# Kernel optimization log

Hardware: AMD Instinct MI355X
Metric: run time of the kernel (lower is better)

## Reference

```python
import jax, jax.numpy as jnp
import numpy as np

G = 32           # number of graphs
NODES = 256      # nodes per graph (equal-sized graphs)
P = 8            # primary capsules per node
IN_DIM = 128     # primary capsule dim
O = 16           # out_caps
OUT_DIM = 128    # out capsule dim
SDIM = OUT_DIM // 2
V = 16           # vector channels
R = 3            # routing iterations


def squash(t, axis=-1):
    sn = jnp.sum(t * t, axis=axis, keepdims=True)
    scale = sn / (1.0 + sn)
    return scale * t / (jnp.sqrt(sn) + 1e-8)


def setup_inputs() -> dict:
    key = jax.random.key(0)
    ks = jax.random.split(key, 4)
    N = G * NODES
    x = jax.random.normal(ks[0], (N, P, IN_DIM), dtype=jnp.float32)
    x_vectors = jax.random.normal(ks[1], (N, V, 3), dtype=jnp.float32)
    W_scalar = jax.random.normal(ks[2], (O, IN_DIM // 2, SDIM), dtype=jnp.float32)
    W_vector = jax.random.normal(ks[3], (O, IN_DIM // 2, OUT_DIM - SDIM), dtype=jnp.float32)
    bias = jnp.zeros((O, OUT_DIM), dtype=jnp.float32)
    batch = jnp.repeat(jnp.arange(G, dtype=jnp.int64), NODES)  # contiguous equal-size graphs
    return {"x": x, "x_vectors": x_vectors, "W_scalar": W_scalar,
            "W_vector": W_vector, "bias": bias, "batch": batch}


def reference(x, x_vectors, W_scalar, W_vector, bias, batch):
    # Equal-size contiguous graphs -> per-graph masking == reshape to [G, NODES, ...]
    xg = x.reshape(G, NODES, P, IN_DIM)
    xvg = x_vectors.reshape(G, NODES, V, 3)

    def per_graph(xb, xvb):
        scalar_part = xb[..., : IN_DIM // 2]           # [n, P, D/2]
        vector_part = xb[..., IN_DIM // 2:]
        u_s = jnp.einsum('npd,ods->npos', scalar_part, W_scalar)
        u_v = jnp.einsum('npd,odv->npov', vector_part, W_vector)
        u = jnp.concatenate([u_s, u_v], axis=-1).reshape(NODES * P, O, OUT_DIM)

        b = jnp.zeros((NODES * P, O), dtype=xb.dtype)
        c = None
        v = None
        for it in range(R):
            c = jax.nn.softmax(b, axis=1)                     # [M, O]
            s_j = jnp.einsum('mo,mod->od', c, u) + bias       # [O, OUT_DIM]
            v = squash(s_j, axis=1)
            if it < R - 1:
                agreement = jnp.einsum('mos,os->mo', u[..., :SDIM], v[:, :SDIM])
                b = b + agreement

        cr = c.reshape(NODES, P, O)
        routed = jnp.einsum('npo,nvc->ovc', cr, xvb)          # [O, V, 3]
        return v, routed

    caps, vecs = jax.vmap(per_graph)(xg, xvg)
    return caps, vecs
```

## Files before the change

kernel.cpp:

```cpp
#include <hip/hip_runtime.h>

#define G_    32
#define O_    16
#define OUTD  128
#define DS_   64
#define VC    48
#define M_    2048
#define ROWS  128
#define CPG   16
#define XP    136
#define XPD   68
#define WVP   72
#define YLP   132

typedef __attribute__((ext_vector_type(8))) short short8;
typedef __attribute__((ext_vector_type(4))) float f32x4;
typedef unsigned long long u64_t;

__device__ __forceinline__ unsigned short f2bf(float f) {
  unsigned u = __float_as_uint(f);
  return (unsigned short)((u + 0x7FFFu + ((u >> 16) & 1u)) >> 16);
}
__device__ __forceinline__ float bf2f(short v) {
  return __uint_as_float(((unsigned)(unsigned short)v) << 16);
}

__device__ __forceinline__ void st8f(float* p, float a, float b) {
  union { float f[2]; u64_t u; } x; x.f[0] = a; x.f[1] = b;
  __hip_atomic_store((u64_t*)p, x.u, __ATOMIC_RELAXED, __HIP_MEMORY_SCOPE_AGENT);
}
__device__ __forceinline__ void ld8f(const float* p, float& a, float& b) {
  union { float f[2]; u64_t u; } x;
  x.u = __hip_atomic_load((const u64_t*)p, __ATOMIC_RELAXED, __HIP_MEMORY_SCOPE_AGENT);
  a = x.f[0]; b = x.f[1];
}

__device__ __forceinline__ void graph_barrier(unsigned* cnt, unsigned target) {
  asm volatile("s_waitcnt vmcnt(0)" ::: "memory");
  __syncthreads();
  if (threadIdx.x == 0) {
    __hip_atomic_fetch_add(cnt, 1u, __ATOMIC_RELAXED, __HIP_MEMORY_SCOPE_AGENT);
    unsigned guard = 0;
    while (__hip_atomic_load(cnt, __ATOMIC_RELAXED, __HIP_MEMORY_SCOPE_AGENT) < target) {
      __builtin_amdgcn_s_sleep(1);
      if (++guard > (1u << 20)) break;
    }
  }
  __syncthreads();
}

__global__ __launch_bounds__(512) void caps_mega(
    const float* __restrict__ x, const float* __restrict__ xv,
    const float* __restrict__ Ws, const float* __restrict__ Wv,
    const float* __restrict__ bias, short* __restrict__ wvacc_bf,
    float* __restrict__ y_part, float* __restrict__ routed_part,
    float* __restrict__ ysum_part, float* __restrict__ caps,
    float* __restrict__ vecs, unsigned* __restrict__ bar)
{
  const int b = blockIdx.x, g = b >> 3, pair = b & 7;
  const int t = threadIdx.x, h = t >> 8, tt = t & 255;
  const int lane = tt & 63, w = tt >> 6;
  const int chunk = pair * 2 + h;
  const int blk_lin = g * CPG + chunk;

  __shared__ short xT[2][128 * XP];
  __shared__ short cT[2][O_ * XP];
  __shared__ short wv_s[O_ * WVP];
  __shared__ float y_lds[2][16 * YLP];
  __shared__ float cp_s[2][16][17];
  __shared__ float xv_s[2][16 * VC];
  __shared__ float yB[2][128];
  __shared__ float vB[2][64];
  __shared__ float pn_s[4];
  __shared__ float wv_acc_s[2][64];

  unsigned* cnt = bar + g * 64;

  {
    const float* xg = x + (size_t)(g * M_ + chunk * ROWS) * OUTD;
    const int rg = tt >> 2, qc = tt & 3;
    const float4* r0q = (const float4*)(xg + (size_t)(2 * rg) * OUTD + qc * 32);
    const float4* r1q = (const float4*)(xg + (size_t)(2 * rg + 1) * OUTD + qc * 32);
    float4 a0 = r0q[0], a1 = r0q[1], a2 = r0q[2], a3 = r0q[3],
           a4 = r0q[4], a5 = r0q[5], a6 = r0q[6], a7 = r0q[7];
    float4 b0 = r1q[0], b1 = r1q[1], b2 = r1q[2], b3 = r1q[3],
           b4 = r1q[4], b5 = r1q[5], b6 = r1q[6], b7 = r1q[7];
    unsigned* xTd = (unsigned*)&xT[h][0];
    const int cb = qc * 32;
#define STAGE4(S, A, B)                                                        \
    xTd[(cb + S*4 + 0) * XPD + rg] = (unsigned)f2bf(A.x) | ((unsigned)f2bf(B.x) << 16); \
    xTd[(cb + S*4 + 1) * XPD + rg] = (unsigned)f2bf(A.y) | ((unsigned)f2bf(B.y) << 16); \
    xTd[(cb + S*4 + 2) * XPD + rg] = (unsigned)f2bf(A.z) | ((unsigned)f2bf(B.z) << 16); \
    xTd[(cb + S*4 + 3) * XPD + rg] = (unsigned)f2bf(A.w) | ((unsigned)f2bf(B.w) << 16);
    STAGE4(0, a0, b0) STAGE4(1, a1, b1) STAGE4(2, a2, b2) STAGE4(3, a3, b3)
    STAGE4(4, a4, b4) STAGE4(5, a5, b5) STAGE4(6, a6, b6) STAGE4(7, a7, b7)
#undef STAGE4
  }
  {
    const float* xvg = xv + (size_t)(g * 256 + chunk * 16) * VC;
    for (int i = tt; i < 16 * VC; i += 256) xv_s[h][i] = xvg[i];
  }
  __syncthreads();
  {
    const int k = tt >> 1, half = tt & 1;
    float s = 0.f;
#pragma unroll
    for (int j = 0; j < 8; ++j) {
      short8 v = *(const short8*)&xT[h][k * XP + half * 64 + j * 8];
#pragma unroll
      for (int e = 0; e < 8; ++e) s += bf2f(v[e]);
    }
    s += __shfl_xor(s, 1);
    float s1 = __shfl_xor(s, 2);
    if ((tt & 3) == 0) st8f(&ysum_part[(size_t)blk_lin * 128 + k], s, s1);
  }
  graph_barrier(cnt, 8);

#define LOGIT_TILE(NT2, CF)                                                    \
    {                                                                          \
      const int nt = 2 * w + NT2;                                              \
      const int mcol = nt * 16 + mrow;                                         \
      f32x4 acc = {0.f, 0.f, 0.f, 0.f};                                        \
      _Pragma("unroll")                                                        \
      for (int ks = 0; ks < 2; ++ks) {                                         \
        short8 af = *(const short8*)&wv_s[mrow * WVP + ks * 32 + gq * 8];      \
        short8 bfr;                                                            \
        _Pragma("unroll")                                                      \
        for (int e = 0; e < 8; ++e)                                            \
          bfr[e] = xT[h][(ks * 32 + gq * 8 + e) * XP + mcol];                  \
        acc = __builtin_amdgcn_mfma_f32_16x16x32_bf16(af, bfr, acc, 0, 0, 0);  \
      }                                                                        \
      float mx = fmaxf(fmaxf(acc[0], acc[1]), fmaxf(acc[2], acc[3]));          \
      mx = fmaxf(mx, __shfl_xor(mx, 16));                                      \
      mx = fmaxf(mx, __shfl_xor(mx, 32));                                      \
      float e0 = __expf(acc[0] - mx), e1 = __expf(acc[1] - mx);                \
      float e2 = __expf(acc[2] - mx), e3 = __expf(acc[3] - mx);                \
      float sm = e0 + e1 + e2 + e3;                                            \
      sm += __shfl_xor(sm, 16);                                                \
      sm += __shfl_xor(sm, 32);                                                \
      float inv = 1.f / sm;                                                    \
      CF[0] = e0 * inv; CF[1] = e1 * inv; CF[2] = e2 * inv; CF[3] = e3 * inv;  \
      cT[h][(gq * 4 + 0) * XP + mcol] = (short)f2bf(CF[0]);                    \
      cT[h][(gq * 4 + 1) * XP + mcol] = (short)f2bf(CF[1]);                    \
      cT[h][(gq * 4 + 2) * XP + mcol] = (short)f2bf(CF[2]);                    \
      cT[h][(gq * 4 + 3) * XP + mcol] = (short)f2bf(CF[3]);                    \
    }

#define CP_TILE(NT2, CF)                                                       \
    {                                                                          \
      const int nt = 2 * w + NT2;                                              \
      _Pragma("unroll")                                                        \
      for (int r = 0; r < 4; ++r) {                                            \
        float v = CF[r];                                                       \
        v += __shfl_xor(v, 1); v += __shfl_xor(v, 2); v += __shfl_xor(v, 4);   \
        if ((lane & 7) == 0)                                                   \
          cp_s[h][nt * 2 + ((lane >> 3) & 1)][gq * 4 + r] = v;                 \
      }                                                                        \
    }

#define A_ROLE(LASTF)                                                          \
  {                                                                            \
    if (t < 256) {                                                             \
      u64_t v4 = __hip_atomic_load(                                            \
          (const u64_t*)&wvacc_bf[(size_t)g * 1024 + t * 4],                   \
          __ATOMIC_RELAXED, __HIP_MEMORY_SCOPE_AGENT);                         \
      const int o = (t * 4) >> 6, k = (t * 4) & 63;                            \
      wv_s[o * WVP + k + 0] = (short)(v4 & 0xFFFF);                            \
      wv_s[o * WVP + k + 1] = (short)((v4 >> 16) & 0xFFFF);                    \
      wv_s[o * WVP + k + 2] = (short)((v4 >> 32) & 0xFFFF);                    \
      wv_s[o * WVP + k + 3] = (short)((v4 >> 48) & 0xFFFF);                    \
    }                                                                          \
    __syncthreads();                                                           \
    { const int mrow = lane & 15, gq = lane >> 4;                              \
      float c_fA[4], c_fB[4];                                                  \
      LOGIT_TILE(0, c_fA)                                                      \
      LOGIT_TILE(1, c_fB)                                                      \
      if (LASTF) { CP_TILE(0, c_fA) CP_TILE(1, c_fB) }                         \
      (void)c_fA; (void)c_fB; }                                                \
    __syncthreads();                                                           \
    { const int oc = lane & 15, gq = lane >> 4;                                \
      f32x4 y0 = {0.f,0.f,0.f,0.f}, y1 = {0.f,0.f,0.f,0.f};                    \
      _Pragma("unroll")                                                        \
      for (int ks = 0; ks < 4; ++ks) {                                         \
        short8 bfv = *(const short8*)&cT[h][oc * XP + ks * 32 + gq * 8];       \
        short8 a0 = *(const short8*)&xT[h][((2*w+0)*16 + oc) * XP + ks*32 + gq*8]; \
        short8 a1 = *(const short8*)&xT[h][((2*w+1)*16 + oc) * XP + ks*32 + gq*8]; \
        y0 = __builtin_amdgcn_mfma_f32_16x16x32_bf16(a0, bfv, y0, 0, 0, 0);    \
        y1 = __builtin_amdgcn_mfma_f32_16x16x32_bf16(a1, bfv, y1, 0, 0, 0);    \
      }                                                                        \
      _Pragma("unroll")                                                        \
      for (int r = 0; r < 4; ++r) {                                            \
        y_lds[h][oc * YLP + (2*w+0) * 16 + gq * 4 + r] = y0[r];                \
        y_lds[h][oc * YLP + (2*w+1) * 16 + gq * 4 + r] = y1[r];                \
      } }                                                                      \
    __syncthreads();                                                           \
    { float* yp = y_part + (size_t)blk_lin * 2048;                             \
      const int oo = tt >> 4, k8 = (tt & 15) * 8;                              \
      const float* sp = &y_lds[h][oo * YLP + k8];                              \
      _Pragma("unroll")                                                        \
      for (int e = 0; e < 4; ++e)                                              \
        st8f(&yp[tt * 8 + 2*e], sp[2*e], sp[2*e + 1]); }                       \
    if (LASTF) {                                                               \
      float* rp = routed_part + (size_t)blk_lin * 768;                         \
      _Pragma("unroll")                                                        \
      for (int e = 0; e < 2; ++e) {                                            \
        const int q = tt + 256 * e;                                            \
        if (q < 384) {                                                         \
          const int idx0 = 2 * q;                                              \
          const int o = idx0 / VC, j = idx0 - o * VC;                          \
          float a0 = 0.f, a1 = 0.f;                                            \
          _Pragma("unroll")                                                    \
          for (int n = 0; n < 16; ++n) {                                       \
            a0 += cp_s[h][n][o] * xv_s[h][n * VC + j];                         \
            a1 += cp_s[h][n][o] * xv_s[h][n * VC + j + 1];                     \
          }                                                                    \
          st8f(&rp[idx0], a0, a1);                                             \
        } } }                                                                  \
  }

#define B_ROLE(FIRSTF, LASTF)                                                  \
  {                                                                            \
    if (FIRSTF) {                                                              \
      if (t < 64) {                                                            \
        float s0 = 0.f, s1 = 0.f;                                              \
        _Pragma("unroll")                                                      \
        for (int ch = 0; ch < CPG; ++ch) {                                     \
          float a, bb;                                                         \
          ld8f(&ysum_part[(size_t)(g * CPG + ch) * 128 + 2 * t], a, bb);       \
          s0 += a; s1 += bb;                                                   \
        }                                                                      \
        s0 *= 0.0625f; s1 *= 0.0625f;                                          \
        yB[0][2*t] = s0; yB[0][2*t+1] = s1;                                    \
        yB[1][2*t] = s0; yB[1][2*t+1] = s1;                                    \
      }                                                                        \
    } else {                                                                   \
      if (t < 128) {                                                           \
        const int o2 = t >> 6, kp = t & 63;                                    \
        const float* yp = y_part + (size_t)g * CPG * 2048 + (pair*2 + o2) * 128 + kp * 2; \
        float s0 = 0.f, s1 = 0.f;                                              \
        _Pragma("unroll")                                                      \
        for (int ch = 0; ch < CPG; ++ch) {                                     \
          float a, bb; ld8f(&yp[ch * 2048], a, bb);                            \
          s0 += a; s1 += bb;                                                   \
        }                                                                      \
        yB[o2][kp*2] = s0; yB[o2][kp*2+1] = s1;                                \
      }                                                                        \
    }                                                                          \
    __syncthreads();                                                           \
    float sv = 0.f;                                                            \
    if (t < 256) {                                                             \
      const int ol = t >> 7, d = t & 127, o = pair * 2 + ol;                   \
      const float* W = (d < 64) ? (Ws + (size_t)o * 4096 + d)                  \
                                : (Wv + (size_t)o * 4096 + (d - 64));          \
      const int kbase = (d < 64) ? 0 : 64;                                     \
      float s = 0.f;                                                           \
      _Pragma("unroll")                                                        \
      for (int k = 0; k < 64; ++k) s += yB[ol][kbase + k] * W[k * 64];         \
      s += bias[o * OUTD + d];                                                 \
      sv = s;                                                                  \
      float pn = s * s;                                                        \
      _Pragma("unroll")                                                        \
      for (int m = 1; m < 64; m <<= 1) pn += __shfl_xor(pn, m);                \
      if ((t & 63) == 0) pn_s[t >> 6] = pn;                                    \
    }                                                                          \
    __syncthreads();                                                           \
    if (t < 256) {                                                             \
      const int ol = t >> 7, d = t & 127, o = pair * 2 + ol;                   \
      float sn = pn_s[ol * 2] + pn_s[ol * 2 + 1];                              \
      float f = sn / ((1.f + sn) * (sqrtf(sn) + 1e-8f));                       \
      float v = f * sv;                                                        \
      if (d < 64) vB[ol][d] = v;                                               \
      if (LASTF) caps[((size_t)g * O_ + o) * OUTD + d] = v;                    \
    }                                                                          \
    __syncthreads();                                                           \
    if (!(LASTF)) {                                                            \
      if (t < 128) {                                                           \
        const int ol2 = t >> 6, k = t & 63, o2 = pair * 2 + ol2;               \
        const float* Wr = Ws + ((size_t)o2 * 64 + k) * 64;                     \
        float acc = 0.f;                                                       \
        _Pragma("unroll")                                                      \
        for (int ss = 0; ss < 64; ss += 4) {                                   \
          float4 wq = *(const float4*)(Wr + ss);                               \
          float4 vq = *(const float4*)&vB[ol2][ss];                            \
          acc += wq.x*vq.x + wq.y*vq.y + wq.z*vq.z + wq.w*vq.w;                \
        }                                                                      \
        wv_acc_s[ol2][k] = ((FIRSTF) ? 0.f : wv_acc_s[ol2][k]) + acc;          \
      }                                                                        \
      __syncthreads();                                                         \
      if (t < 32) {                                                            \
        const int ol2 = t >> 4, k = (t & 15) * 4;                              \
        u64_t v4 =  (u64_t)(unsigned short)f2bf(wv_acc_s[ol2][k + 0])          \
                 | ((u64_t)(unsigned short)f2bf(wv_acc_s[ol2][k + 1]) << 16)   \
                 | ((u64_t)(unsigned short)f2bf(wv_acc_s[ol2][k + 2]) << 32)   \
                 | ((u64_t)(unsigned short)f2bf(wv_acc_s[ol2][k + 3]) << 48);  \
        __hip_atomic_store(                                                    \
            (u64_t*)&wvacc_bf[(size_t)g * 1024 + (pair * 2 + ol2) * 64 + k],   \
            v4, __ATOMIC_RELAXED, __HIP_MEMORY_SCOPE_AGENT);                   \
      }                                                                        \
    } else {                                                                   \
      if (t < 48) {                                                            \
        const int idx = pair * 96 + 2 * t;                                     \
        const float* rp = routed_part + (size_t)g * CPG * 768 + idx;           \
        float s0 = 0.f, s1 = 0.f;                                              \
        _Pragma("unroll")                                                      \
        for (int ch = 0; ch < CPG; ++ch) {                                     \
          float a, bb; ld8f(&rp[ch * 768], a, bb);                             \
          s0 += a; s1 += bb;                                                   \
        }                                                                      \
        vecs[(size_t)g * 768 + idx] = s0;                                      \
        vecs[(size_t)g * 768 + idx + 1] = s1;                                  \
      }                                                                        \
    }                                                                          \
  }

  B_ROLE(1, 0)
  graph_barrier(cnt, 16);
  A_ROLE(0)
  graph_barrier(cnt, 24);
  B_ROLE(0, 0)
  graph_barrier(cnt, 32);
  A_ROLE(1)
  graph_barrier(cnt, 40);
  B_ROLE(0, 1)

#undef A_ROLE
#undef B_ROLE
#undef LOGIT_TILE
#undef CP_TILE
}

extern "C" void kernel_launch(void* const* d_in, const int* in_sizes, int n_in,
                              void* d_out, int out_size, void* d_ws, size_t ws_size,
                              hipStream_t stream)
{
  const float* x    = (const float*)d_in[0];
  const float* xv   = (const float*)d_in[1];
  const float* Ws   = (const float*)d_in[2];
  const float* Wv   = (const float*)d_in[3];
  const float* bias = (const float*)d_in[4];

  float* out  = (float*)d_out;
  float* caps = out;
  float* vecs = out + (size_t)G_ * O_ * OUTD;

  float* ws          = (float*)d_ws;
  unsigned* bar      = (unsigned*)ws;
  float* ysum_part   = ws + 4096;
  float* y_part      = ysum_part + (size_t)G_ * CPG * 128;
  float* routed_part = y_part + (size_t)G_ * CPG * 2048;
  short* wvacc_bf    = (short*)(routed_part + (size_t)G_ * CPG * 768);

  hipMemsetAsync((void*)bar, 0, (size_t)G_ * 64 * sizeof(unsigned), stream);
  caps_mega<<<dim3(G_ * 8), dim3(512), 0, stream>>>(
      x, xv, Ws, Wv, bias, wvacc_bf, y_part, routed_part, ysum_part,
      caps, vecs, bar);
}
```

Before: 43.38 us.

## Use one block per row chunk and output capsule, doubling grid to 512 blocks

Changes the work split from 256 blocks that each handled two row chunks and two output capsules, one per 256-thread half, to 512 blocks of 512 threads that each handle one chunk and one capsule. The logits and y MFMA tiles are divided over 8 waves instead of 2 tiles per wave, and the B-role matvecs split the K dimension across thread halves with an LDS partial-sum reduce. This raises parallelism and shrinks shared memory per block, but each graph barrier now waits on 16 blocks, and more blocks must all be co-resident for the spin barriers to make progress.

After: 40.89 us. -5.7%, faster.

```diff
diff --git a/kernel.cpp b/kernel.cpp
--- a/kernel.cpp
+++ b/kernel.cpp
@@ -49,7 +49,7 @@
   __syncthreads();
 }
 
-__global__ __launch_bounds__(512) void caps_mega(
+__global__ __launch_bounds__(512) void caps_mega2(
     const float* __restrict__ x, const float* __restrict__ xv,
     const float* __restrict__ Ws, const float* __restrict__ Wv,
     const float* __restrict__ bias, short* __restrict__ wvacc_bf,
@@ -57,68 +57,79 @@
     float* __restrict__ ysum_part, float* __restrict__ caps,
     float* __restrict__ vecs, unsigned* __restrict__ bar)
 {
-  const int b = blockIdx.x, g = b >> 3, pair = b & 7;
+  const int b = blockIdx.x, g = b >> 4, chunk = b & 15;
   const int t = threadIdx.x, h = t >> 8, tt = t & 255;
-  const int lane = tt & 63, w = tt >> 6;
-  const int chunk = pair * 2 + h;
-  const int blk_lin = g * CPG + chunk;
-
-  __shared__ short xT[2][128 * XP];
-  __shared__ short cT[2][O_ * XP];
+  const int lane = t & 63, w = t >> 6;
+
+  __shared__ short xT[128 * XP];
+  __shared__ short cT[O_ * XP];
   __shared__ short wv_s[O_ * WVP];
-  __shared__ float y_lds[2][16 * YLP];
-  __shared__ float cp_s[2][16][17];
-  __shared__ float xv_s[2][16 * VC];
-  __shared__ float yB[2][128];
-  __shared__ float vB[2][64];
-  __shared__ float pn_s[4];
-  __shared__ float wv_acc_s[2][64];
+  __shared__ float y_lds[16 * YLP];
+  __shared__ float cp_s[16][17];
+  __shared__ float xv_s[16 * VC];
+  __shared__ float yB[128];
+  __shared__ float ps[2][128];
+  __shared__ float vB[64];
+  __shared__ float pn_s[2];
+  __shared__ float wv_acc_s[64];
 
   unsigned* cnt = bar + g * 64;
 
   {
-    const float* xg = x + (size_t)(g * M_ + chunk * ROWS) * OUTD;
+    const float* xg = x + (size_t)b * (ROWS * OUTD);
     const int rg = tt >> 2, qc = tt & 3;
-    const float4* r0q = (const float4*)(xg + (size_t)(2 * rg) * OUTD + qc * 32);
-    const float4* r1q = (const float4*)(xg + (size_t)(2 * rg + 1) * OUTD + qc * 32);
-    float4 a0 = r0q[0], a1 = r0q[1], a2 = r0q[2], a3 = r0q[3],
-           a4 = r0q[4], a5 = r0q[5], a6 = r0q[6], a7 = r0q[7];
-    float4 b0 = r1q[0], b1 = r1q[1], b2 = r1q[2], b3 = r1q[3],
-           b4 = r1q[4], b5 = r1q[5], b6 = r1q[6], b7 = r1q[7];
-    unsigned* xTd = (unsigned*)&xT[h][0];
-    const int cb = qc * 32;
+    const float* r0 = xg + (size_t)(2 * rg) * OUTD + qc * 32 + h * 16;
+    const float* r1 = r0 + OUTD;
+    const float4* r0q = (const float4*)r0;
+    const float4* r1q = (const float4*)r1;
+    float4 a0 = r0q[0], a1 = r0q[1], a2 = r0q[2], a3 = r0q[3];
+    float4 b0 = r1q[0], b1 = r1q[1], b2 = r1q[2], b3 = r1q[3];
+    unsigned* xTd = (unsigned*)xT;
+    const int cb = qc * 32 + h * 16;
 #define STAGE4(S, A, B)                                                        \
     xTd[(cb + S*4 + 0) * XPD + rg] = (unsigned)f2bf(A.x) | ((unsigned)f2bf(B.x) << 16); \
     xTd[(cb + S*4 + 1) * XPD + rg] = (unsigned)f2bf(A.y) | ((unsigned)f2bf(B.y) << 16); \
     xTd[(cb + S*4 + 2) * XPD + rg] = (unsigned)f2bf(A.z) | ((unsigned)f2bf(B.z) << 16); \
     xTd[(cb + S*4 + 3) * XPD + rg] = (unsigned)f2bf(A.w) | ((unsigned)f2bf(B.w) << 16);
     STAGE4(0, a0, b0) STAGE4(1, a1, b1) STAGE4(2, a2, b2) STAGE4(3, a3, b3)
-    STAGE4(4, a4, b4) STAGE4(5, a5, b5) STAGE4(6, a6, b6) STAGE4(7, a7, b7)
 #undef STAGE4
   }
   {
     const float* xvg = xv + (size_t)(g * 256 + chunk * 16) * VC;
-    for (int i = tt; i < 16 * VC; i += 256) xv_s[h][i] = xvg[i];
+    for (int i = t; i < 16 * VC; i += 512) xv_s[i] = xvg[i];
   }
   __syncthreads();
-  {
+  if (h == 0) {
     const int k = tt >> 1, half = tt & 1;
     float s = 0.f;
 #pragma unroll
     for (int j = 0; j < 8; ++j) {
-      short8 v = *(const short8*)&xT[h][k * XP + half * 64 + j * 8];
+      short8 v = *(const short8*)&xT[k * XP + half * 64 + j * 8];
 #pragma unroll
       for (int e = 0; e < 8; ++e) s += bf2f(v[e]);
     }
     s += __shfl_xor(s, 1);
     float s1 = __shfl_xor(s, 2);
-    if ((tt & 3) == 0) st8f(&ysum_part[(size_t)blk_lin * 128 + k], s, s1);
-  }
-  graph_barrier(cnt, 8);
-
-#define LOGIT_TILE(NT2, CF)                                                    \
-    {                                                                          \
-      const int nt = 2 * w + NT2;                                              \
+    if ((tt & 3) == 0) st8f(&ysum_part[(size_t)b * 128 + k], s, s1);
+  }
+  graph_barrier(cnt, 16);
+
+#define A_ROLE(LASTF)                                                          \
+  {                                                                            \
+    if (t < 256) {                                                             \
+      u64_t v4 = __hip_atomic_load(                                            \
+          (const u64_t*)&wvacc_bf[(size_t)g * 1024 + t * 4],                   \
+          __ATOMIC_RELAXED, __HIP_MEMORY_SCOPE_AGENT);                         \
+      const int o = t >> 4, k = (t * 4) & 63;                                  \
+      wv_s[o * WVP + k + 0] = (short)(v4 & 0xFFFF);                            \
+      wv_s[o * WVP + k + 1] = (short)((v4 >> 16) & 0xFFFF);                    \
+      wv_s[o * WVP + k + 2] = (short)((v4 >> 32) & 0xFFFF);                    \
+      wv_s[o * WVP + k + 3] = (short)((v4 >> 48) & 0xFFFF);                    \
+    }                                                                          \
+    __syncthreads();                                                           \
+                               \
+    { const int mrow = lane & 15, gq = lane >> 4;                              \
+      const int nt = w;                                                        \
       const int mcol = nt * 16 + mrow;                                         \
       f32x4 acc = {0.f, 0.f, 0.f, 0.f};                                        \
       _Pragma("unroll")                                                        \
@@ -127,7 +138,7 @@
         short8 bfr;                                                            \
         _Pragma("unroll")                                                      \
         for (int e = 0; e < 8; ++e)                                            \
-          bfr[e] = xT[h][(ks * 32 + gq * 8 + e) * XP + mcol];                  \
+          bfr[e] = xT[(ks * 32 + gq * 8 + e) * XP + mcol];                     \
         acc = __builtin_amdgcn_mfma_f32_16x16x32_bf16(af, bfr, acc, 0, 0, 0);  \
       }                                                                        \
       float mx = fmaxf(fmaxf(acc[0], acc[1]), fmaxf(acc[2], acc[3]));          \
@@ -139,90 +150,61 @@
       sm += __shfl_xor(sm, 16);                                                \
       sm += __shfl_xor(sm, 32);                                                \
       float inv = 1.f / sm;                                                    \
-      CF[0] = e0 * inv; CF[1] = e1 * inv; CF[2] = e2 * inv; CF[3] = e3 * inv;  \
-      cT[h][(gq * 4 + 0) * XP + mcol] = (short)f2bf(CF[0]);                    \
-      cT[h][(gq * 4 + 1) * XP + mcol] = (short)f2bf(CF[1]);                    \
-      cT[h][(gq * 4 + 2) * XP + mcol] = (short)f2bf(CF[2]);                    \
-      cT[h][(gq * 4 + 3) * XP + mcol] = (short)f2bf(CF[3]);                    \
-    }
-
-#define CP_TILE(NT2, CF)                                                       \
-    {                                                                          \
-      const int nt = 2 * w + NT2;                                              \
-      _Pragma("unroll")                                                        \
-      for (int r = 0; r < 4; ++r) {                                            \
-        float v = CF[r];                                                       \
-        v += __shfl_xor(v, 1); v += __shfl_xor(v, 2); v += __shfl_xor(v, 4);   \
-        if ((lane & 7) == 0)                                                   \
-          cp_s[h][nt * 2 + ((lane >> 3) & 1)][gq * 4 + r] = v;                 \
-      }                                                                        \
-    }
-
-#define A_ROLE(LASTF)                                                          \
-  {                                                                            \
-    if (t < 256) {                                                             \
-      u64_t v4 = __hip_atomic_load(                                            \
-          (const u64_t*)&wvacc_bf[(size_t)g * 1024 + t * 4],                   \
-          __ATOMIC_RELAXED, __HIP_MEMORY_SCOPE_AGENT);                         \
-      const int o = (t * 4) >> 6, k = (t * 4) & 63;                            \
-      wv_s[o * WVP + k + 0] = (short)(v4 & 0xFFFF);                            \
-      wv_s[o * WVP + k + 1] = (short)((v4 >> 16) & 0xFFFF);                    \
-      wv_s[o * WVP + k + 2] = (short)((v4 >> 32) & 0xFFFF);                    \
-      wv_s[o * WVP + k + 3] = (short)((v4 >> 48) & 0xFFFF);                    \
-    }                                                                          \
-    __syncthreads();                                                           \
-    { const int mrow = lane & 15, gq = lane >> 4;                              \
-      float c_fA[4], c_fB[4];                                                  \
-      LOGIT_TILE(0, c_fA)                                                      \
-      LOGIT_TILE(1, c_fB)                                                      \
-      if (LASTF) { CP_TILE(0, c_fA) CP_TILE(1, c_fB) }                         \
-      (void)c_fA; (void)c_fB; }                                                \
-    __syncthreads();                                                           \
+      float c0 = e0 * inv, c1 = e1 * inv, c2 = e2 * inv, c3 = e3 * inv;        \
+      cT[(gq * 4 + 0) * XP + mcol] = (short)f2bf(c0);                          \
+      cT[(gq * 4 + 1) * XP + mcol] = (short)f2bf(c1);                          \
+      cT[(gq * 4 + 2) * XP + mcol] = (short)f2bf(c2);                          \
+      cT[(gq * 4 + 3) * XP + mcol] = (short)f2bf(c3);                          \
+      if (LASTF) {                                                             \
+        float cf[4] = {c0, c1, c2, c3};                                        \
+        _Pragma("unroll")                                                      \
+        for (int r = 0; r < 4; ++r) {                                          \
+          float v = cf[r];                                                     \
+          v += __shfl_xor(v, 1); v += __shfl_xor(v, 2); v += __shfl_xor(v, 4); \
+          if ((lane & 7) == 0)                                                 \
+            cp_s[nt * 2 + ((lane >> 3) & 1)][gq * 4 + r] = v;                  \
+        }                                                                      \
+      } }                                                                      \
+    __syncthreads();                                                           \
+                                              \
     { const int oc = lane & 15, gq = lane >> 4;                                \
-      f32x4 y0 = {0.f,0.f,0.f,0.f}, y1 = {0.f,0.f,0.f,0.f};                    \
+      f32x4 y0 = {0.f,0.f,0.f,0.f};                                            \
       _Pragma("unroll")                                                        \
       for (int ks = 0; ks < 4; ++ks) {                                         \
-        short8 bfv = *(const short8*)&cT[h][oc * XP + ks * 32 + gq * 8];       \
-        short8 a0 = *(const short8*)&xT[h][((2*w+0)*16 + oc) * XP + ks*32 + gq*8]; \
-        short8 a1 = *(const short8*)&xT[h][((2*w+1)*16 + oc) * XP + ks*32 + gq*8]; \
-        y0 = __builtin_amdgcn_mfma_f32_16x16x32_bf16(a0, bfv, y0, 0, 0, 0);    \
-        y1 = __builtin_amdgcn_mfma_f32_16x16x32_bf16(a1, bfv, y1, 0, 0, 0);    \
-      }                                                                        \
-      _Pragma("unroll")                                                        \
-      for (int r = 0; r < 4; ++r) {                                            \
-        y_lds[h][oc * YLP + (2*w+0) * 16 + gq * 4 + r] = y0[r];                \
-        y_lds[h][oc * YLP + (2*w+1) * 16 + gq * 4 + r] = y1[r];                \
+        short8 bfv = *(const short8*)&cT[oc * XP + ks * 32 + gq * 8];          \
+        short8 av = *(const short8*)&xT[(w * 16 + oc) * XP + ks * 32 + gq * 8];\
+        y0 = __builtin_amdgcn_mfma_f32_16x16x32_bf16(av, bfv, y0, 0, 0, 0);    \
+      }                                                                        \
+      _Pragma("unroll")                                                        \
+      for (int r = 0; r < 4; ++r)                                              \
+        y_lds[oc * YLP + w * 16 + gq * 4 + r] = y0[r]; }                       \
+    __syncthreads();                                                           \
+    { float* yp = y_part + (size_t)b * 2048;                                   \
+      const int oo = t >> 5, kk = (t * 4) & 127;                               \
+      const float* sp = &y_lds[oo * YLP + kk];                                 \
+      st8f(&yp[t * 4], sp[0], sp[1]);                                          \
+      st8f(&yp[t * 4 + 2], sp[2], sp[3]); }                                    \
+    if (LASTF) {                                                               \
+      if (t < 384) {                                                           \
+        float* rp = routed_part + (size_t)b * 768;                             \
+        const int idx0 = 2 * t;                                                \
+        const int o = idx0 / VC, j = idx0 - o * VC;                            \
+        float a0 = 0.f, a1 = 0.f;                                              \
+        _Pragma("unroll")                                                      \
+        for (int n = 0; n < 16; ++n) {                                         \
+          a0 += cp_s[n][o] * xv_s[n * VC + j];                                 \
+          a1 += cp_s[n][o] * xv_s[n * VC + j + 1];                             \
+        }                                                                      \
+        st8f(&rp[idx0], a0, a1);                                               \
       } }                                                                      \
-    __syncthreads();                                                           \
-    { float* yp = y_part + (size_t)blk_lin * 2048;                             \
-      const int oo = tt >> 4, k8 = (tt & 15) * 8;                              \
-      const float* sp = &y_lds[h][oo * YLP + k8];                              \
-      _Pragma("unroll")                                                        \
-      for (int e = 0; e < 4; ++e)                                              \
-        st8f(&yp[tt * 8 + 2*e], sp[2*e], sp[2*e + 1]); }                       \
-    if (LASTF) {                                                               \
-      float* rp = routed_part + (size_t)blk_lin * 768;                         \
-      _Pragma("unroll")                                                        \
-      for (int e = 0; e < 2; ++e) {                                            \
-        const int q = tt + 256 * e;                                            \
-        if (q < 384) {                                                         \
-          const int idx0 = 2 * q;                                              \
-          const int o = idx0 / VC, j = idx0 - o * VC;                          \
-          float a0 = 0.f, a1 = 0.f;                                            \
-          _Pragma("unroll")                                                    \
-          for (int n = 0; n < 16; ++n) {                                       \
-            a0 += cp_s[h][n][o] * xv_s[h][n * VC + j];                         \
-            a1 += cp_s[h][n][o] * xv_s[h][n * VC + j + 1];                     \
-          }                                                                    \
-          st8f(&rp[idx0], a0, a1);                                             \
-        } } }                                                                  \
   }
 
 #define B_ROLE(FIRSTF, LASTF)                                                  \
   {                                                                            \
-    if (FIRSTF) {                                                              \
-      if (t < 64) {                                                            \
-        float s0 = 0.f, s1 = 0.f;                                              \
+    const int o = chunk;                                                       \
+    if (t < 64) {                                                              \
+      float s0 = 0.f, s1 = 0.f;                                                \
+      if (FIRSTF) {                                                            \
         _Pragma("unroll")                                                      \
         for (int ch = 0; ch < CPG; ++ch) {                                     \
           float a, bb;                                                         \
@@ -230,76 +212,78 @@
           s0 += a; s1 += bb;                                                   \
         }                                                                      \
         s0 *= 0.0625f; s1 *= 0.0625f;                                          \
-        yB[0][2*t] = s0; yB[0][2*t+1] = s1;                                    \
-        yB[1][2*t] = s0; yB[1][2*t+1] = s1;                                    \
-      }                                                                        \
-    } else {                                                                   \
-      if (t < 128) {                                                           \
-        const int o2 = t >> 6, kp = t & 63;                                    \
-        const float* yp = y_part + (size_t)g * CPG * 2048 + (pair*2 + o2) * 128 + kp * 2; \
-        float s0 = 0.f, s1 = 0.f;                                              \
+      } else {                                                                 \
+        const float* yp = y_part + (size_t)g * CPG * 2048 + o * 128 + 2 * t;   \
         _Pragma("unroll")                                                      \
         for (int ch = 0; ch < CPG; ++ch) {                                     \
           float a, bb; ld8f(&yp[ch * 2048], a, bb);                            \
           s0 += a; s1 += bb;                                                   \
         }                                                                      \
-        yB[o2][kp*2] = s0; yB[o2][kp*2+1] = s1;                                \
-      }                                                                        \
-    }                                                                          \
-    __syncthreads();                                                           \
-    float sv = 0.f;                                                            \
-    if (t < 256) {                                                             \
-      const int ol = t >> 7, d = t & 127, o = pair * 2 + ol;                   \
+      }                                                                        \
+      yB[2*t] = s0; yB[2*t+1] = s1;                                            \
+    }                                                                          \
+    __syncthreads();                                                           \
+    if (t < 256) {                  \
+      const int kh = t >> 7, d = t & 127;                                      \
       const float* W = (d < 64) ? (Ws + (size_t)o * 4096 + d)                  \
                                 : (Wv + (size_t)o * 4096 + (d - 64));          \
-      const int kbase = (d < 64) ? 0 : 64;                                     \
-      float s = 0.f;                                                           \
-      _Pragma("unroll")                                                        \
-      for (int k = 0; k < 64; ++k) s += yB[ol][kbase + k] * W[k * 64];         \
-      s += bias[o * OUTD + d];                                                 \
-      sv = s;                                                                  \
-      float pn = s * s;                                                        \
+      const int ybase = (d < 64) ? 0 : 64;                                     \
+      float a0 = 0.f, a1 = 0.f;                                                \
+      _Pragma("unroll")                                                        \
+      for (int k = 0; k < 32; k += 2) {                                        \
+        const int kl = kh * 32 + k;                                            \
+        a0 += yB[ybase + kl] * W[(size_t)kl * 64];                             \
+        a1 += yB[ybase + kl + 1] * W[(size_t)(kl + 1) * 64];                   \
+      }                                                                        \
+      ps[kh][d] = a0 + a1;                                                     \
+    }                                                                          \
+    __syncthreads();                                                           \
+    float sv = 0.f;                                                            \
+    if (t < 128) {                                                             \
+      sv = ps[0][t] + ps[1][t] + bias[o * OUTD + t];                           \
+      float pn = sv * sv;                                                      \
       _Pragma("unroll")                                                        \
       for (int m = 1; m < 64; m <<= 1) pn += __shfl_xor(pn, m);                \
       if ((t & 63) == 0) pn_s[t >> 6] = pn;                                    \
     }                                                                          \
     __syncthreads();                                                           \
-    if (t < 256) {                                                             \
-      const int ol = t >> 7, d = t & 127, o = pair * 2 + ol;                   \
-      float sn = pn_s[ol * 2] + pn_s[ol * 2 + 1];                              \
+    if (t < 128) {                                                             \
+      float sn = pn_s[0] + pn_s[1];                                            \
       float f = sn / ((1.f + sn) * (sqrtf(sn) + 1e-8f));                       \
       float v = f * sv;                                                        \
-      if (d < 64) vB[ol][d] = v;                                               \
-      if (LASTF) caps[((size_t)g * O_ + o) * OUTD + d] = v;                    \
+      if (t < 64) vB[t] = v;                                                   \
+      if (LASTF) caps[((size_t)g * O_ + o) * OUTD + t] = v;                    \
     }                                                                          \
     __syncthreads();                                                           \
     if (!(LASTF)) {                                                            \
-      if (t < 128) {                                                           \
-        const int ol2 = t >> 6, k = t & 63, o2 = pair * 2 + ol2;               \
-        const float* Wr = Ws + ((size_t)o2 * 64 + k) * 64;                     \
+      if (t < 128) {          \
+        const int k = t >> 1, half = t & 1;                                    \
+        const float* Wr = Ws + ((size_t)o * 64 + k) * 64 + half * 32;          \
         float acc = 0.f;                                                       \
         _Pragma("unroll")                                                      \
-        for (int ss = 0; ss < 64; ss += 4) {                                   \
+        for (int ss = 0; ss < 32; ss += 4) {                                   \
           float4 wq = *(const float4*)(Wr + ss);                               \
-          float4 vq = *(const float4*)&vB[ol2][ss];                            \
+          float4 vq = *(const float4*)&vB[half * 32 + ss];                     \
           acc += wq.x*vq.x + wq.y*vq.y + wq.z*vq.z + wq.w*vq.w;                \
         }                                                                      \
-        wv_acc_s[ol2][k] = ((FIRSTF) ? 0.f : wv_acc_s[ol2][k]) + acc;          \
+        acc += __shfl_xor(acc, 1);                                             \
+        if (half == 0)                                                         \
+          wv_acc_s[k] = ((FIRSTF) ? 0.f : wv_acc_s[k]) + acc;                  \
       }                                                                        \
       __syncthreads();                                                         \
-      if (t < 32) {                                                            \
-        const int ol2 = t >> 4, k = (t & 15) * 4;                              \
-        u64_t v4 =  (u64_t)(unsigned short)f2bf(wv_acc_s[ol2][k + 0])          \
-                 | ((u64_t)(unsigned short)f2bf(wv_acc_s[ol2][k + 1]) << 16)   \
-                 | ((u64_t)(unsigned short)f2bf(wv_acc_s[ol2][k + 2]) << 32)   \
-                 | ((u64_t)(unsigned short)f2bf(wv_acc_s[ol2][k + 3]) << 48);  \
+      if (t < 16) {     \
+        const int k = t * 4;                                                   \
+        u64_t v4 =  (u64_t)(unsigned short)f2bf(wv_acc_s[k + 0])               \
+                 | ((u64_t)(unsigned short)f2bf(wv_acc_s[k + 1]) << 16)        \
+                 | ((u64_t)(unsigned short)f2bf(wv_acc_s[k + 2]) << 32)        \
+                 | ((u64_t)(unsigned short)f2bf(wv_acc_s[k + 3]) << 48);       \
         __hip_atomic_store(                                                    \
-            (u64_t*)&wvacc_bf[(size_t)g * 1024 + (pair * 2 + ol2) * 64 + k],   \
+            (u64_t*)&wvacc_bf[(size_t)g * 1024 + o * 64 + k],                  \
             v4, __ATOMIC_RELAXED, __HIP_MEMORY_SCOPE_AGENT);                   \
       }                                                                        \
     } else {                                                                   \
-      if (t < 48) {                                                            \
-        const int idx = pair * 96 + 2 * t;                                     \
+      if (t < 24) {                                                            \
+        const int idx = o * VC + 2 * t;                                        \
         const float* rp = routed_part + (size_t)g * CPG * 768 + idx;           \
         float s0 = 0.f, s1 = 0.f;                                              \
         _Pragma("unroll")                                                      \
@@ -314,19 +298,17 @@
   }
 
   B_ROLE(1, 0)
-  graph_barrier(cnt, 16);
+  graph_barrier(cnt, 32);
   A_ROLE(0)
-  graph_barrier(cnt, 24);
+  graph_barrier(cnt, 48);
   B_ROLE(0, 0)
-  graph_barrier(cnt, 32);
+  graph_barrier(cnt, 64);
   A_ROLE(1)
-  graph_barrier(cnt, 40);
+  graph_barrier(cnt, 80);
   B_ROLE(0, 1)
 
 #undef A_ROLE
 #undef B_ROLE
-#undef LOGIT_TILE
-#undef CP_TILE
 }
 
 extern "C" void kernel_launch(void* const* d_in, const int* in_sizes, int n_in,
@@ -351,7 +333,7 @@
   short* wvacc_bf    = (short*)(routed_part + (size_t)G_ * CPG * 768);
 
   hipMemsetAsync((void*)bar, 0, (size_t)G_ * 64 * sizeof(unsigned), stream);
-  caps_mega<<<dim3(G_ * 8), dim3(512), 0, stream>>>(
+  caps_mega2<<<dim3(G_ * CPG), dim3(512), 0, stream>>>(
       x, xv, Ws, Wv, bias, wvacc_bf, y_part, routed_part, ysum_part,
       caps, vecs, bar);
 }
```
